# Optimization experiments

Measured on AMD Instinct MI355X. Metric: run time of the kernel, lower is better.

## Reference

```python
import jax, jax.numpy as jnp
import numpy as np

EMBED_DIM = 768
SCALE = float(np.sqrt(EMBED_DIM / 9.0))


def setup_inputs() -> dict:
    key = jax.random.key(0)
    ks = jax.random.split(key, 7)
    D = EMBED_DIM
    s = 1.0 / np.sqrt(D)
    x = jax.random.normal(ks[0], (8, 2048, D), dtype=jnp.float32)
    Wq = jax.random.uniform(ks[1], (D, D), jnp.float32, -s, s)
    bq = jax.random.uniform(ks[2], (D,), jnp.float32, -s, s)
    Wk = jax.random.uniform(ks[3], (D, D), jnp.float32, -s, s)
    bk = jax.random.uniform(ks[4], (D,), jnp.float32, -s, s)
    Wv = jax.random.uniform(ks[5], (D, D), jnp.float32, -s, s)
    bv = jax.random.uniform(ks[6], (D,), jnp.float32, -s, s)
    return {"x": x, "Wq": Wq, "bq": bq, "Wk": Wk, "bk": bk, "Wv": Wv, "bv": bv}


def reference(x, Wq, bq, Wk, bk, Wv, bv):
    # nn.Linear: y = x @ W^T + b
    Q = jnp.einsum('bnd,ed->bne', x, Wq) + bq
    K = jnp.einsum('bnd,ed->bne', x, Wk) + bk
    V = jnp.einsum('bnd,ed->bne', x, Wv) + bv
    scores = jnp.einsum('bqd,bkd->bqk', Q, K) / SCALE  # [B, Nq, Nk]
    # NOTE: softmax over the QUERY axis (dim=-2), per the original module
    weights = jax.nn.softmax(scores, axis=-2)
    out = jnp.einsum('bqk,bkd->bqd', weights, V)
    return out + x
```

## Files before the change

kernel.cpp:

```cpp
#include <hip/hip_runtime.h>
#include <stdint.h>

#define B_ 8
#define N_ 2048
#define D_ 768

typedef unsigned short u16;
typedef unsigned int u32;
typedef __attribute__((ext_vector_type(8))) short bf16x8;
typedef __attribute__((ext_vector_type(8))) unsigned short u16x8;
typedef __attribute__((ext_vector_type(4))) float f32x4;

static constexpr float INV_SCALE = 0.10825317547305482f;

__device__ __forceinline__ u16 f2bf(float f) {
  union { float f; unsigned u; } v; v.f = f;
  return (u16)((v.u + 0x7FFFu + ((v.u >> 16) & 1u)) >> 16);
}
__device__ __forceinline__ float bf2f(u16 h) {
  union { unsigned u; float f; } v; v.u = ((unsigned)h) << 16;
  return v.f;
}
__device__ __forceinline__ f32x4 mfma16(bf16x8 a, bf16x8 b, f32x4 c) {
  return __builtin_amdgcn_mfma_f32_16x16x32_bf16(a, b, c, 0, 0, 0);
}
__device__ __forceinline__ void gl_lds16(const u16* g, u16* l) {
  __builtin_amdgcn_global_load_lds(
      (const __attribute__((address_space(1))) u32*)g,
      (__attribute__((address_space(3))) u32*)l, 16, 0, 0);
}

__global__ __launch_bounds__(256) void cast_kernel(
    const float* __restrict__ x, const float* __restrict__ wq,
    const float* __restrict__ wk, const float* __restrict__ wv,
    u16* __restrict__ xb, u16* __restrict__ wqb,
    u16* __restrict__ wkb, u16* __restrict__ wvb) {
  const long NX = (long)B_ * N_ * D_;
  const long NW = (long)D_ * D_;
  long i = ((long)blockIdx.x * 256 + threadIdx.x) * 8;
  const float* src; u16* dst; long off;
  if (i < NX) { src = x; dst = xb; off = i; }
  else {
    long j = i - NX;
    int seg = (int)(j / NW);
    off = j - (long)seg * NW;
    src = seg == 0 ? wq : (seg == 1 ? wk : wv);
    dst = seg == 0 ? wqb : (seg == 1 ? wkb : wvb);
  }
  float4 a = *(const float4*)(src + off);
  float4 b = *(const float4*)(src + off + 4);
  u16x8 o;
  o[0]=f2bf(a.x); o[1]=f2bf(a.y); o[2]=f2bf(a.z); o[3]=f2bf(a.w);
  o[4]=f2bf(b.x); o[5]=f2bf(b.y); o[6]=f2bf(b.z); o[7]=f2bf(b.w);
  *(u16x8*)(dst + off) = o;
}

template<int NT>
__device__ __forceinline__ void gemm256(
    const u16* __restrict__ Ag, long lda,
    const u16* __restrict__ Bg, long ldb,
    f32x4 (&acc)[8][4]) {
  __shared__ u16 Ab[2][16384];
  __shared__ u16 Bb[2][16384];
  const int t_ = threadIdx.x, l = t_ & 63, w = t_ >> 6;
  const int lr = l & 15, kq = l >> 4;
  const int wm = w >> 2, wn = w & 3;
  const int arow = wm * 128, brow = wn * 64;

  const int s_rowl = l >> 3;
  const int s_sl = (l & 7) ^ (l >> 3);
  auto STAGE_A = [&](u16* As, int kt) {
    #pragma unroll
    for (int j = 0; j < 4; ++j) {
      const int row = j * 64 + w * 8 + s_rowl;
      gl_lds16(Ag + (long)row * lda + kt * 64 + s_sl * 8,
               As + ((j * 8192 + w * 1024) >> 1));
    }
  };
  auto STAGE_B = [&](u16* Bs, int kt) {
    #pragma unroll
    for (int j = 0; j < 4; ++j) {
      const int row = j * 64 + w * 8 + s_rowl;
      gl_lds16(Bg + (long)row * ldb + kt * 64 + s_sl * 8,
               Bs + ((j * 8192 + w * 1024) >> 1));
    }
  };

#define TILE(XA, XB, YA, YB, kt, DOST)                                       \
  {                                                                          \
    if (DOST) {                                                              \
      STAGE_A(YA, (kt) + 1);                                                 \
      asm volatile("s_waitcnt vmcnt(4)" ::: "memory");                       \
    } else {                                                                 \
      asm volatile("s_waitcnt vmcnt(0)" ::: "memory");                       \
    }                                                                        \
    __builtin_amdgcn_s_barrier();                                            \
    asm volatile("" ::: "memory");                                           \
    bf16x8 bf[4][2];                                                         \
    _Pragma("unroll")                                                        \
    for (int nf = 0; nf < 4; ++nf) {                                         \
      const int row = brow + nf * 16 + lr;                                   \
      _Pragma("unroll")                                                      \
      for (int ks = 0; ks < 2; ++ks)                                         \
        bf[nf][ks] = *(const bf16x8*)(XB + row * 64 +                        \
                        (((4 * ks + kq) ^ (lr & 7)) * 8));                   \
    }                                                                        \
    {                                                                        \
      bf16x8 af[4][2];                                                       \
      _Pragma("unroll")                                                      \
      for (int mf = 0; mf < 4; ++mf) {                                       \
        const int row = arow + mf * 16 + lr;                                 \
        _Pragma("unroll")                                                    \
        for (int ks = 0; ks < 2; ++ks)                                       \
          af[mf][ks] = *(const bf16x8*)(XA + row * 64 +                      \
                          (((4 * ks + kq) ^ (lr & 7)) * 8));                 \
      }                                                                      \
      __builtin_amdgcn_s_setprio(1);                                         \
      _Pragma("unroll")                                                      \
      for (int ks = 0; ks < 2; ++ks)                                         \
        _Pragma("unroll")                                                    \
        for (int mf = 0; mf < 4; ++mf)                                       \
          _Pragma("unroll")                                                  \
          for (int nf = 0; nf < 4; ++nf)                                     \
            acc[mf][nf] = mfma16(af[mf][ks], bf[nf][ks], acc[mf][nf]);       \
      __builtin_amdgcn_s_setprio(0);                                         \
    }                                                                        \
    if (DOST) STAGE_B(YB, (kt) + 1);                                         \
    {                                                                        \
      bf16x8 af[4][2];                                                       \
      _Pragma("unroll")                                                      \
      for (int mf = 0; mf < 4; ++mf) {                                       \
        const int row = arow + 64 + mf * 16 + lr;                            \
        _Pragma("unroll")                                                    \
        for (int ks = 0; ks < 2; ++ks)                                       \
          af[mf][ks] = *(const bf16x8*)(XA + row * 64 +                      \
                          (((4 * ks + kq) ^ (lr & 7)) * 8));                 \
      }                                                                      \
      __builtin_amdgcn_s_setprio(1);                                         \
      _Pragma("unroll")                                                      \
      for (int ks = 0; ks < 2; ++ks)                                         \
        _Pragma("unroll")                                                    \
        for (int mf = 0; mf < 4; ++mf)                                       \
          _Pragma("unroll")                                                  \
          for (int nf = 0; nf < 4; ++nf)                                     \
            acc[4 + mf][nf] = mfma16(af[mf][ks], bf[nf][ks], acc[4 + mf][nf]); \
      __builtin_amdgcn_s_setprio(0);                                         \
    }                                                                        \
    asm volatile("" ::: "memory");                                           \
    __builtin_amdgcn_s_barrier();                                            \
  }

  STAGE_A(Ab[0], 0);
  STAGE_B(Bb[0], 0);
  for (int t2 = 0; t2 < NT; t2 += 2) {
    TILE(Ab[0], Bb[0], Ab[1], Bb[1], t2, true)
    TILE(Ab[1], Bb[1], Ab[0], Bb[0], t2 + 1, (t2 + 2 < NT))
  }
#undef TILE
}

__global__ __launch_bounds__(512, 2) void qkv_gemm(
    const u16* __restrict__ xb,
    const u16* __restrict__ wq, const u16* __restrict__ wk, const u16* __restrict__ wv,
    const float* __restrict__ bq, const float* __restrict__ bk, const float* __restrict__ bv,
    u16* __restrict__ Qs, u16* __restrict__ Kb, u16* __restrict__ Vb) {
  const int lin = blockIdx.x;
  const int xcd = lin & 7, inner = lin >> 3;
  const int rt = xcd * 8 + (inner & 7);
  const int rest = inner >> 3;
  const int ct = rest % 3, mat = rest / 3;
  const u16* W = mat == 0 ? wq : (mat == 1 ? wk : wv);
  const float* bias = mat == 0 ? bq : (mat == 1 ? bk : bv);
  u16* out = mat == 0 ? Qs : (mat == 1 ? Kb : Vb);
  const float scl = mat == 0 ? INV_SCALE : 1.0f;
  const int rbase = rt * 256, cbase = ct * 256;

  f32x4 acc[8][4] = {};
  gemm256<D_ / 64>(xb + (long)rbase * D_, D_, W + (long)cbase * D_, D_, acc);

  const int l = threadIdx.x & 63, w = threadIdx.x >> 6;
  const int lr = l & 15, orow = (l >> 4) * 4;
  const int wm = w >> 2, wn = w & 3;
  #pragma unroll
  for (int mf = 0; mf < 8; ++mf)
    #pragma unroll
    for (int nf = 0; nf < 4; ++nf) {
      int col = cbase + wn * 64 + nf * 16 + lr;
      float bc = bias[col];
      #pragma unroll
      for (int r = 0; r < 4; ++r) {
        int row = rbase + wm * 128 + mf * 16 + orow + r;
        out[(long)row * D_ + col] = f2bf((acc[mf][nf][r] + bc) * scl);
      }
    }
}

__global__ __launch_bounds__(512, 2) void qk_exp(
    const u16* __restrict__ Qs, const u16* __restrict__ Kb,
    u16* __restrict__ P, float* __restrict__ denpart) {
  const int lin = blockIdx.x;
  const int b = lin & 7, inner = lin >> 3;
  const int kblk = inner & 7, qblk = inner >> 3;

  f32x4 acc[8][4] = {};
  gemm256<D_ / 64>(Qs + ((long)b * N_ + qblk * 256) * D_, D_,
                   Kb + ((long)b * N_ + kblk * 256) * D_, D_, acc);

  const int tt = threadIdx.x, l = tt & 63, w = tt >> 6;
  const int lr = l & 15, orow = (l >> 4) * 4;
  const int wm = w >> 2, wn = w & 3;
  float csum[4] = {0.f, 0.f, 0.f, 0.f};
  #pragma unroll
  for (int mf = 0; mf < 8; ++mf)
    #pragma unroll
    for (int nf = 0; nf < 4; ++nf) {
      long kk = kblk * 256 + wn * 64 + nf * 16 + lr;
      #pragma unroll
      for (int r = 0; r < 4; ++r) {
        long q = qblk * 256 + wm * 128 + mf * 16 + orow + r;
        float e = __expf(acc[mf][nf][r]);
        u16 pe = f2bf(e);
        P[((long)b * N_ + q) * N_ + kk] = pe;
        csum[nf] += bf2f(pe);
      }
    }
  #pragma unroll
  for (int nf = 0; nf < 4; ++nf) {
    csum[nf] += __shfl_xor(csum[nf], 16);
    csum[nf] += __shfl_xor(csum[nf], 32);
  }
  if (l < 16) {
    #pragma unroll
    for (int nf = 0; nf < 4; ++nf)
      denpart[((long)(qblk * 2 + wm) * B_ + b) * N_ +
              kblk * 256 + wn * 64 + nf * 16 + l] = csum[nf];
  }
}

__global__ __launch_bounds__(256) void scale_transpose(
    const u16* __restrict__ Vb, const float* __restrict__ denpart,
    u16* __restrict__ VsT) {
  const int b = blockIdx.z, k0 = blockIdx.y * 64, d0 = blockIdx.x * 64;
  __shared__ float tile[64][65];
  __shared__ float invden[64];
  const int t = threadIdx.x;
  if (t < 64) {
    float s = 0.f;
    for (int qs = 0; qs < 16; ++qs)
      s += denpart[((long)qs * B_ + b) * N_ + k0 + t];
    invden[t] = 1.0f / s;
  }
  __syncthreads();
  for (int idx = t; idx < 4096; idx += 256) {
    int kl = idx >> 6, dl = idx & 63;
    float v = bf2f(Vb[((long)b * N_ + k0 + kl) * D_ + d0 + dl]) * invden[kl];
    tile[dl][kl] = v;
  }
  __syncthreads();
  for (int idx = t; idx < 4096; idx += 256) {
    int dl = idx >> 6, kl = idx & 63;
    VsT[((long)b * D_ + d0 + dl) * N_ + k0 + kl] = f2bf(tile[dl][kl]);
  }
}

__global__ __launch_bounds__(512, 2) void pv_gemm(
    const u16* __restrict__ P, const u16* __restrict__ VsT,
    const u16* __restrict__ xb, float* __restrict__ out) {
  const int lin = blockIdx.x;
  const int b = lin & 7, inner = lin >> 3;
  const int qt = inner % 8, dt = inner / 8;
  const int q0 = qt * 256, d0 = dt * 256;

  f32x4 acc[8][4] = {};
  gemm256<N_ / 64>(P + ((long)b * N_ + q0) * N_, N_,
                   VsT + ((long)b * D_ + d0) * N_, N_, acc);

  const int l = threadIdx.x & 63, w = threadIdx.x >> 6;
  const int lr = l & 15, orow = (l >> 4) * 4;
  const int wm = w >> 2, wn = w & 3;
  #pragma unroll
  for (int mf = 0; mf < 8; ++mf)
    #pragma unroll
    for (int nf = 0; nf < 4; ++nf) {
      int dd = d0 + wn * 64 + nf * 16 + lr;
      #pragma unroll
      for (int r = 0; r < 4; ++r) {
        int q = q0 + wm * 128 + mf * 16 + orow + r;
        long idx = ((long)b * N_ + q) * D_ + dd;
        out[idx] = acc[mf][nf][r] + bf2f(xb[idx]);
      }
    }
}

extern "C" void kernel_launch(void* const* d_in, const int* in_sizes, int n_in,
                              void* d_out, int out_size, void* d_ws, size_t ws_size,
                              hipStream_t stream) {
  const float* x  = (const float*)d_in[0];
  const float* Wq = (const float*)d_in[1];
  const float* bq = (const float*)d_in[2];
  const float* Wk = (const float*)d_in[3];
  const float* bk = (const float*)d_in[4];
  const float* Wv = (const float*)d_in[5];
  const float* bv = (const float*)d_in[6];

  char* ws = (char*)d_ws;
  u16* xb  = (u16*)(ws + 0);
  u16* wqb = (u16*)(ws + 25165824);
  u16* wkb = (u16*)(ws + 26345472);
  u16* wvb = (u16*)(ws + 27525120);
  u16* Qs  = (u16*)(ws + 28704768);
  u16* Kb  = (u16*)(ws + 53870592);
  u16* Vb  = (u16*)(ws + 79036416);
  u16* VsT = (u16*)(ws + 104202240);
  u16* P   = (u16*)(ws + 129368064);
  float* denpart = (float*)(ws + 196476928);
  (void)in_sizes; (void)n_in; (void)out_size; (void)ws_size;

  cast_kernel<<<7008, 256, 0, stream>>>(x, Wq, Wk, Wv, xb, wqb, wkb, wvb);
  qkv_gemm<<<576, 512, 0, stream>>>(xb, wqb, wkb, wvb, bq, bk, bv, Qs, Kb, Vb);
  qk_exp<<<512, 512, 0, stream>>>(Qs, Kb, P, denpart);
  scale_transpose<<<dim3(12, 32, 8), 256, 0, stream>>>(Vb, denpart, VsT);
  pv_gemm<<<192, 512, 0, stream>>>(P, VsT, xb, (float*)d_out);
}
```

Baseline: 221.0 us.

## Store P and scaled V in FP8 and run PV GEMM with FP8 MFMA

The softmax numerator matrix P and the transposed, normalised V are now stored as FP8 (e4m3) instead of bf16, and the PV GEMM uses a new FP8 MFMA tile loop with its own LDS staging and swizzle. V is scaled up by a constant before quantisation and scaled back in the epilogue to stay inside FP8 range. The aim is to halve the bytes of the large P intermediate written and read, and to use the higher-throughput FP8 MFMA. The cost is lower precision in the attention product, which could push the output past the accuracy tolerance.

```diff
diff --git a/kernel.cpp b/kernel.cpp
--- a/kernel.cpp
+++ b/kernel.cpp
@@ -6,12 +6,14 @@
 #define D_ 768
 
 typedef unsigned short u16;
+typedef unsigned char u8;
 typedef unsigned int u32;
 typedef __attribute__((ext_vector_type(8))) short bf16x8;
 typedef __attribute__((ext_vector_type(8))) unsigned short u16x8;
 typedef __attribute__((ext_vector_type(4))) float f32x4;
 
 static constexpr float INV_SCALE = 0.10825317547305482f;
+static constexpr float VS_SCALE = 4096.0f;
 
 __device__ __forceinline__ u16 f2bf(float f) {
   union { float f; unsigned u; } v; v.f = f;
@@ -21,10 +23,24 @@
   union { unsigned u; float f; } v; v.u = ((unsigned)h) << 16;
   return v.f;
 }
+__device__ __forceinline__ u8 f2fp8(float f) {
+  union { float f; u32 u; } v; v.f = f;
+  u32 s = (v.u >> 24) & 0x80u;
+  u32 m = v.u & 0x7fffffffu;
+  if (m >= 0x43E00000u) return (u8)(s | 0x7Eu);
+  if (m < 0x3C800000u) return (u8)s;
+  m += 0x000FFFFFu + ((m >> 20) & 1u);
+  int e = (int)(m >> 23) - 127;
+  if (e > 8) return (u8)(s | 0x7Eu);
+  return (u8)(s | ((u32)(e + 7) << 3) | ((m >> 20) & 7u));
+}
 __device__ __forceinline__ f32x4 mfma16(bf16x8 a, bf16x8 b, f32x4 c) {
   return __builtin_amdgcn_mfma_f32_16x16x32_bf16(a, b, c, 0, 0, 0);
 }
-__device__ __forceinline__ void gl_lds16(const u16* g, u16* l) {
+__device__ __forceinline__ f32x4 mfma8(long a, long b, f32x4 c) {
+  return __builtin_amdgcn_mfma_f32_16x16x32_fp8_fp8(a, b, c, 0, 0, 0);
+}
+__device__ __forceinline__ void gl_lds16(const void* g, void* l) {
   __builtin_amdgcn_global_load_lds(
       (const __attribute__((address_space(1))) u32*)g,
       (__attribute__((address_space(3))) u32*)l, 16, 0, 0);
@@ -66,7 +82,6 @@
   const int lr = l & 15, kq = l >> 4;
   const int wm = w >> 2, wn = w & 3;
   const int arow = wm * 128, brow = wn * 64;
-
   const int s_rowl = l >> 3;
   const int s_sl = (l & 7) ^ (l >> 3);
   auto STAGE_A = [&](u16* As, int kt) {
@@ -157,6 +172,110 @@
     TILE(Ab[1], Bb[1], Ab[0], Bb[0], t2 + 1, (t2 + 2 < NT))
   }
 #undef TILE
+}
+
+template<int NT>
+__device__ __forceinline__ void gemm256_fp8(
+    const u8* __restrict__ Ag, long lda,
+    const u8* __restrict__ Bg, long ldb,
+    f32x4 (&acc)[8][4]) {
+  __shared__ u8 Ab[2][16384];
+  __shared__ u8 Bb[2][16384];
+  const int t_ = threadIdx.x, l = t_ & 63, w = t_ >> 6;
+  const int lr = l & 15, kq = l >> 4;
+  const int wm = w >> 2, wn = w & 3;
+  const int arow = wm * 128, brow = wn * 64;
+  const int srow_l = l >> 2;
+  const int s16src = (l & 3) ^ ((l >> 2) & 3);
+  auto STAGE_A = [&](u8* As, int kt) {
+    #pragma unroll
+    for (int c = 0; c < 2; ++c) {
+      const int ch = w * 2 + c;
+      gl_lds16(Ag + (long)(ch * 16 + srow_l) * lda + kt * 64 + s16src * 16,
+               As + ch * 1024);
+    }
+  };
+  auto STAGE_B = [&](u8* Bs, int kt) {
+    #pragma unroll
+    for (int c = 0; c < 2; ++c) {
+      const int ch = w * 2 + c;
+      gl_lds16(Bg + (long)(ch * 16 + srow_l) * ldb + kt * 64 + s16src * 16,
+               Bs + ch * 1024);
+    }
+  };
+#define FR8(BASE, ROW, KS)                                                   \
+  (*(const long*)((BASE) + (ROW) * 64 +                                      \
+      ((((4 * (KS) + kq) >> 1) ^ ((ROW) & 3)) * 16) + ((4 * (KS) + kq) & 1) * 8))
+
+#define TILE8(XA, XB, YA, YB, kt, DOST)                                      \
+  {                                                                          \
+    if (DOST) {                                                              \
+      STAGE_A(YA, (kt) + 1);                                                 \
+      asm volatile("s_waitcnt vmcnt(2)" ::: "memory");                       \
+    } else {                                                                 \
+      asm volatile("s_waitcnt vmcnt(0)" ::: "memory");                       \
+    }                                                                        \
+    __builtin_amdgcn_s_barrier();                                            \
+    asm volatile("" ::: "memory");                                           \
+    long bfr[4][2];                                                          \
+    _Pragma("unroll")                                                        \
+    for (int nf = 0; nf < 4; ++nf) {                                         \
+      const int row = brow + nf * 16 + lr;                                   \
+      _Pragma("unroll")                                                      \
+      for (int ks = 0; ks < 2; ++ks)                                         \
+        bfr[nf][ks] = FR8(XB, row, ks);                                      \
+    }                                                                        \
+    {                                                                        \
+      long afr[4][2];                                                        \
+      _Pragma("unroll")                                                      \
+      for (int mf = 0; mf < 4; ++mf) {                                       \
+        const int row = arow + mf * 16 + lr;                                 \
+        _Pragma("unroll")                                                    \
+        for (int ks = 0; ks < 2; ++ks)                                       \
+          afr[mf][ks] = FR8(XA, row, ks);                                    \
+      }                                                                      \
+      __builtin_amdgcn_s_setprio(1);                                         \
+      _Pragma("unroll")                                                      \
+      for (int ks = 0; ks < 2; ++ks)                                         \
+        _Pragma("unroll")                                                    \
+        for (int mf = 0; mf < 4; ++mf)                                       \
+          _Pragma("unroll")                                                  \
+          for (int nf = 0; nf < 4; ++nf)                                     \
+            acc[mf][nf] = mfma8(afr[mf][ks], bfr[nf][ks], acc[mf][nf]);      \
+      __builtin_amdgcn_s_setprio(0);                                         \
+    }                                                                        \
+    if (DOST) STAGE_B(YB, (kt) + 1);                                         \
+    {                                                                        \
+      long afr[4][2];                                                        \
+      _Pragma("unroll")                                                      \
+      for (int mf = 0; mf < 4; ++mf) {                                       \
+        const int row = arow + 64 + mf * 16 + lr;                            \
+        _Pragma("unroll")                                                    \
+        for (int ks = 0; ks < 2; ++ks)                                       \
+          afr[mf][ks] = FR8(XA, row, ks);                                    \
+      }                                                                      \
+      __builtin_amdgcn_s_setprio(1);                                         \
+      _Pragma("unroll")                                                      \
+      for (int ks = 0; ks < 2; ++ks)                                         \
+        _Pragma("unroll")                                                    \
+        for (int mf = 0; mf < 4; ++mf)                                       \
+          _Pragma("unroll")                                                  \
+          for (int nf = 0; nf < 4; ++nf)                                     \
+            acc[4 + mf][nf] = mfma8(afr[mf][ks], bfr[nf][ks], acc[4 + mf][nf]); \
+      __builtin_amdgcn_s_setprio(0);                                         \
+    }                                                                        \
+    asm volatile("" ::: "memory");                                           \
+    __builtin_amdgcn_s_barrier();                                            \
+  }
+
+  STAGE_A(Ab[0], 0);
+  STAGE_B(Bb[0], 0);
+  for (int t2 = 0; t2 < NT; t2 += 2) {
+    TILE8(Ab[0], Bb[0], Ab[1], Bb[1], t2, true)
+    TILE8(Ab[1], Bb[1], Ab[0], Bb[0], t2 + 1, (t2 + 2 < NT))
+  }
+#undef TILE8
+#undef FR8
 }
 
 __global__ __launch_bounds__(512, 2) void qkv_gemm(
@@ -197,7 +316,7 @@
 
 __global__ __launch_bounds__(512, 2) void qk_exp(
     const u16* __restrict__ Qs, const u16* __restrict__ Kb,
-    u16* __restrict__ P, float* __restrict__ denpart) {
+    u8* __restrict__ P8, float* __restrict__ denpart) {
   const int lin = blockIdx.x;
   const int b = lin & 7, inner = lin >> 3;
   const int kblk = inner & 7, qblk = inner >> 3;
@@ -219,9 +338,8 @@
       for (int r = 0; r < 4; ++r) {
         long q = qblk * 256 + wm * 128 + mf * 16 + orow + r;
         float e = __expf(acc[mf][nf][r]);
-        u16 pe = f2bf(e);
-        P[((long)b * N_ + q) * N_ + kk] = pe;
-        csum[nf] += bf2f(pe);
+        P8[((long)b * N_ + q) * N_ + kk] = f2fp8(e);
+        csum[nf] += e;
       }
     }
   #pragma unroll
@@ -239,7 +357,7 @@
 
 __global__ __launch_bounds__(256) void scale_transpose(
     const u16* __restrict__ Vb, const float* __restrict__ denpart,
-    u16* __restrict__ VsT) {
+    u8* __restrict__ VsT8) {
   const int b = blockIdx.z, k0 = blockIdx.y * 64, d0 = blockIdx.x * 64;
   __shared__ float tile[64][65];
   __shared__ float invden[64];
@@ -248,7 +366,7 @@
     float s = 0.f;
     for (int qs = 0; qs < 16; ++qs)
       s += denpart[((long)qs * B_ + b) * N_ + k0 + t];
-    invden[t] = 1.0f / s;
+    invden[t] = VS_SCALE / s;
   }
   __syncthreads();
   for (int idx = t; idx < 4096; idx += 256) {
@@ -259,12 +377,12 @@
   __syncthreads();
   for (int idx = t; idx < 4096; idx += 256) {
     int dl = idx >> 6, kl = idx & 63;
-    VsT[((long)b * D_ + d0 + dl) * N_ + k0 + kl] = f2bf(tile[dl][kl]);
+    VsT8[((long)b * D_ + d0 + dl) * N_ + k0 + kl] = f2fp8(tile[dl][kl]);
   }
 }
 
 __global__ __launch_bounds__(512, 2) void pv_gemm(
-    const u16* __restrict__ P, const u16* __restrict__ VsT,
+    const u8* __restrict__ P8, const u8* __restrict__ VsT8,
     const u16* __restrict__ xb, float* __restrict__ out) {
   const int lin = blockIdx.x;
   const int b = lin & 7, inner = lin >> 3;
@@ -272,12 +390,13 @@
   const int q0 = qt * 256, d0 = dt * 256;
 
   f32x4 acc[8][4] = {};
-  gemm256<N_ / 64>(P + ((long)b * N_ + q0) * N_, N_,
-                   VsT + ((long)b * D_ + d0) * N_, N_, acc);
+  gemm256_fp8<N_ / 64>(P8 + ((long)b * N_ + q0) * N_, N_,
+                       VsT8 + ((long)b * D_ + d0) * N_, N_, acc);
 
   const int l = threadIdx.x & 63, w = threadIdx.x >> 6;
   const int lr = l & 15, orow = (l >> 4) * 4;
   const int wm = w >> 2, wn = w & 3;
+  const float inv_s = 1.0f / VS_SCALE;
   #pragma unroll
   for (int mf = 0; mf < 8; ++mf)
     #pragma unroll
@@ -287,7 +406,7 @@
       for (int r = 0; r < 4; ++r) {
         int q = q0 + wm * 128 + mf * 16 + orow + r;
         long idx = ((long)b * N_ + q) * D_ + dd;
-        out[idx] = acc[mf][nf][r] + bf2f(xb[idx]);
+        out[idx] = acc[mf][nf][r] * inv_s + bf2f(xb[idx]);
       }
     }
 }
@@ -311,14 +430,14 @@
   u16* Qs  = (u16*)(ws + 28704768);
   u16* Kb  = (u16*)(ws + 53870592);
   u16* Vb  = (u16*)(ws + 79036416);
-  u16* VsT = (u16*)(ws + 104202240);
-  u16* P   = (u16*)(ws + 129368064);
+  u8*  VsT8 = (u8*)(ws + 104202240);
+  u8*  P8   = (u8*)(ws + 129368064);
   float* denpart = (float*)(ws + 196476928);
   (void)in_sizes; (void)n_in; (void)out_size; (void)ws_size;
 
   cast_kernel<<<7008, 256, 0, stream>>>(x, Wq, Wk, Wv, xb, wqb, wkb, wvb);
   qkv_gemm<<<576, 512, 0, stream>>>(xb, wqb, wkb, wvb, bq, bk, bv, Qs, Kb, Vb);
-  qk_exp<<<512, 512, 0, stream>>>(Qs, Kb, P, denpart);
-  scale_transpose<<<dim3(12, 32, 8), 256, 0, stream>>>(Vb, denpart, VsT);
-  pv_gemm<<<192, 512, 0, stream>>>(P, VsT, xb, (float*)d_out);
-}
+  qk_exp<<<512, 512, 0, stream>>>(Qs, Kb, P8, denpart);
+  scale_transpose<<<dim3(12, 32, 8), 256, 0, stream>>>(Vb, denpart, VsT8);
+  pv_gemm<<<192, 512, 0, stream>>>(P8, VsT8, xb, (float*)d_out);
+}
```

Result: slower. 247.6 us (+12.0%).
